# Kernel tuning notes

Measured on AMD Instinct MI355X. Metric: run time of the kernel, lower is better.

Reference implementation:

```python
import jax, jax.numpy as jnp
import numpy as np

D_MODEL = 1024
N_HEADS = 16
D_V = D_MODEL // N_HEADS  # 64


def setup_inputs() -> dict:
    key = jax.random.key(0)
    k1, k2, k3, k4, k5, k6 = jax.random.split(key, 6)
    N, L = 2, 2048
    return {
        "queries": jax.random.normal(k1, (N, L, D_MODEL), jnp.float32),
        "keys": jax.random.normal(k2, (N, L, D_MODEL), jnp.float32),
        "values": jax.random.normal(k3, (N, L, D_MODEL), jnp.float32),
        # key-padding mask, 0 = masked out (broadcast over heads and queries)
        "mask": jax.random.randint(k4, (N, 1, 1, L), 0, 2).astype(jnp.int32),
        # torch nn.Linear(d_model, d_model): weight [out, in], bias [out]
        "fc_w": jax.random.normal(k5, (D_MODEL, D_MODEL), jnp.float32) / np.sqrt(D_MODEL).astype(np.float32),
        "fc_b": jax.random.normal(k6, (D_MODEL,), jnp.float32) * 0.01,
    }


def reference(queries, keys, values, mask, fc_w, fc_b):
    N, Lq, _ = queries.shape
    Lk = keys.shape[1]
    # NOTE: the source defines Q/K/V Linear layers but never applies them in forward.
    q = queries.reshape(N, Lq, N_HEADS, D_V).transpose(0, 2, 1, 3)  # [N,H,Lq,Dv]
    k = keys.reshape(N, Lk, N_HEADS, D_V)                            # [N,Lk,H,Dv]
    v = values.reshape(N, Lk, N_HEADS, D_V)                          # [N,Lk,H,Dv]
    energy = jnp.einsum('nhqd,nkhd->nhqk', q, k)                     # QK^T
    energy = jnp.where(mask == 0, -jnp.inf, energy)                  # masked_fill
    # faithful to source: scale by sqrt(d_model), applied after masking
    attn = jax.nn.softmax(energy / jnp.sqrt(jnp.float32(D_MODEL)), axis=-1)
    out = jnp.einsum('nhqk,nkhd->nqhd', attn, v).reshape(N, Lq, N_HEADS * D_V)
    return out @ fc_w.T + fc_b
```

## Files before the change

### kernel.cpp

```cpp
#include <hip/hip_runtime.h>
#include <hip/hip_bf16.h>

#define SEQL 2048
#define DMODEL 1024

typedef short bf16x8 __attribute__((ext_vector_type(8)));
typedef short bf16x4 __attribute__((ext_vector_type(4)));
typedef float f32x4 __attribute__((ext_vector_type(4)));
typedef unsigned short u16;

__device__ __forceinline__ u16 f2bf(float f) {
    union { float f; unsigned u; } v; v.f = f;
    unsigned r = v.u + 0x7FFFu + ((v.u >> 16) & 1u);
    return (u16)(r >> 16);
}

__device__ __forceinline__ void async16(u16* lds, const u16* g) {
    __builtin_amdgcn_global_load_lds(
        (const __attribute__((address_space(1))) unsigned int*)g,
        (__attribute__((address_space(3))) unsigned int*)lds,
        16, 0, 0);
}


#define TSTR 72

__global__ __launch_bounds__(256) void pack_all(
    const float* __restrict__ kg, const float* __restrict__ wg,
    const float* __restrict__ vg, const int* __restrict__ mg,
    u16* __restrict__ kb, u16* __restrict__ wb, u16* __restrict__ vtb,
    float* __restrict__ maskf)
{
    __shared__ __align__(16) u16 T[64 * TSTR];
    const int b = blockIdx.x, t = threadIdx.x;
    u16 o[8];
    if (b < 2048) {
        const int e0 = (b * 256 + t) * 8;
        const int n = e0 >> 21;
        const int s = (e0 >> 10) & 2047;
        const int dm = e0 & 1023, h = dm >> 6, d0 = dm & 63;
        const float4 x0 = *(const float4*)(kg + e0);
        const float4 x1 = *(const float4*)(kg + e0 + 4);
        o[0]=f2bf(x0.x); o[1]=f2bf(x0.y); o[2]=f2bf(x0.z); o[3]=f2bf(x0.w);
        o[4]=f2bf(x1.x); o[5]=f2bf(x1.y); o[6]=f2bf(x1.z); o[7]=f2bf(x1.w);
        const int kt = s >> 6, st = (s >> 4) & 3, m = s & 15;
        const int f = d0 >> 5, qd = (d0 >> 3) & 3;
        u16* dst = kb + ((size_t)((n * 16 + h) * 32 + kt)) * 4096
                      + (st * 2 + f) * 512 + (m + 16 * qd) * 8;
        *(bf16x8*)dst = *(bf16x8*)o;
    } else if (b < 2560) {
        const int e0 = ((b - 2048) * 256 + t) * 8;
        const int col = e0 >> 10, k0 = e0 & 1023;
        const float4 x0 = *(const float4*)(wg + e0);
        const float4 x1 = *(const float4*)(wg + e0 + 4);
        o[0]=f2bf(x0.x); o[1]=f2bf(x0.y); o[2]=f2bf(x0.z); o[3]=f2bf(x0.w);
        o[4]=f2bf(x1.x); o[5]=f2bf(x1.y); o[6]=f2bf(x1.z); o[7]=f2bf(x1.w);
        const int cb = col >> 6, cj = (col >> 4) & 3, m = col & 15;
        const int kt = k0 >> 6, f = (k0 >> 5) & 1, qd = (k0 >> 3) & 3;
        u16* dst = wb + ((size_t)((cb * 16 + kt) * 8 + cj * 2 + f)) * 512
                      + (m + 16 * qd) * 8;
        *(bf16x8*)dst = *(bf16x8*)o;
    } else if (b < 3584) {
        const int bb = b - 2560;
        const int kt = bb & 31, h = (bb >> 5) & 15, n = bb >> 9;
        {
            const int s = t >> 2, d0 = (t & 3) * 16;
            const float* src = vg + ((size_t)(n * SEQL + kt * 64 + s) * DMODEL) + h * 64 + d0;
            u16 w16[16];
            #pragma unroll
            for (int j = 0; j < 16; ++j) w16[j] = f2bf(src[j]);
            *(bf16x8*)&T[s * TSTR + d0]     = *(bf16x8*)&w16[0];
            *(bf16x8*)&T[s * TSTR + d0 + 8] = *(bf16x8*)&w16[8];
        }
        __syncthreads();
        {
            const int d = t >> 2, k0 = (t & 3) * 16;
            u16 w16[16];
            #pragma unroll
            for (int j = 0; j < 16; ++j) w16[j] = T[(k0 + j) * TSTR + d];
            const int t4 = d >> 4, dr = d & 15;
            u16* base = vtb + ((size_t)((n * 16 + h) * 32 + kt)) * 4096;
            #pragma unroll
            for (int g = 0; g < 2; ++g) {
                const int key0 = k0 + g * 8;
                const int kk = key0 >> 5, qk = (key0 >> 3) & 3;
                *(bf16x8*)(base + (t4 * 2 + kk) * 512 + (dr + 16 * qk) * 8)
                    = *(bf16x8*)&w16[g * 8];
            }
        }
    } else {
        #pragma unroll
        for (int i = 0; i < 16; ++i) {
            const int idx = t * 16 + i;
            maskf[idx] = mg[idx] ? 0.0f : -1.0e5f;
        }
    }
}

#define OSPLIT 4194304
#define LSPLIT 65536

template<int NSPLIT>
__global__ __launch_bounds__(256) void attn_kernel(
    const float* __restrict__ qg, const u16* __restrict__ kb,
    const u16* __restrict__ vtb, const float* __restrict__ maskf,
    u16* __restrict__ xb, float* __restrict__ opart, float* __restrict__ lpart)
{
    __shared__ __align__(16) u16 SM[16384];
    u16* const K_lds = SM;
    u16* const V_lds = SM + 4096;
    u16* const P_lds = SM + 8192;

    const int blk = blockIdx.x;
    const int qblk = blk & 15;
    const int h = (blk >> 4) & 15;
    const int n = (blk >> 8) & 1;
    const int split = blk >> 9;
    const int tid = threadIdx.x;
    const int wave = tid >> 6, lane = tid & 63;
    const int lrow = lane & 15, quad = lane >> 4;
    const int q0 = qblk * 128;

    bf16x8 qf[2][2];
    #pragma unroll
    for (int qi = 0; qi < 2; ++qi) {
        const float* qp = qg + ((size_t)(n * SEQL + q0 + wave * 32 + qi * 16 + lrow) * DMODEL) + h * 64 + quad * 8;
        #pragma unroll
        for (int f = 0; f < 2; ++f) {
            const float4 a = *(const float4*)(qp + f * 32);
            const float4 c = *(const float4*)(qp + f * 32 + 4);
            u16* dst = (u16*)&qf[qi][f];
            dst[0]=f2bf(a.x); dst[1]=f2bf(a.y); dst[2]=f2bf(a.z); dst[3]=f2bf(a.w);
            dst[4]=f2bf(c.x); dst[5]=f2bf(c.y); dst[6]=f2bf(c.z); dst[7]=f2bf(c.w);
        }
    }

    bf16x8 onesf;
    #pragma unroll
    for (int j = 0; j < 8; ++j) ((u16*)&onesf)[j] = 0x3F80;

    f32x4 oacc[2][4];
    f32x4 lacc[2];
    #pragma unroll
    for (int qi = 0; qi < 2; ++qi) {
        lacc[qi] = (f32x4){0.f, 0.f, 0.f, 0.f};
        #pragma unroll
        for (int t4 = 0; t4 < 4; ++t4) oacc[qi][t4] = (f32x4){0.f, 0.f, 0.f, 0.f};
    }

    const u16* ksrc0 = kb  + ((size_t)(n * 16 + h)) * 131072;
    const u16* vsrc0 = vtb + ((size_t)(n * 16 + h)) * 131072;
    const float* mrow = maskf + n * SEQL;

    const int ktlo = split * (32 / NSPLIT);
    const int kthi = ktlo + (32 / NSPLIT);

    for (int kt = ktlo; kt < kthi; ++kt) {
        __syncthreads();
        {
            const u16* ks = ksrc0 + (size_t)kt * 4096;
            const u16* vs = vsrc0 + (size_t)kt * 4096;
            #pragma unroll
            for (int i = 0; i < 2; ++i) {
                const int ch = tid + i * 256;
                async16(&K_lds[ch * 8], ks + ch * 8);
                async16(&V_lds[ch * 8], vs + ch * 8);
            }
        }
        __syncthreads();

        #pragma unroll
        for (int st = 0; st < 4; ++st) {
            const bf16x8 kf0 = *(const bf16x8*)&K_lds[(st * 2 + 0) * 512 + lane * 8];
            const bf16x8 kf1 = *(const bf16x8*)&K_lds[(st * 2 + 1) * 512 + lane * 8];
            const f32x4 mv = *(const f32x4*)&mrow[kt * 64 + st * 16 + quad * 4];
            const int kk = st >> 1;
            const int qk = (st & 1) * 2 + (quad >> 1);
            const int j0 = (quad & 1) * 4;
            #pragma unroll
            for (int qi = 0; qi < 2; ++qi) {
                f32x4 sa = (f32x4){0.f, 0.f, 0.f, 0.f};
                sa = __builtin_amdgcn_mfma_f32_16x16x32_bf16(kf0, qf[qi][0], sa, 0, 0, 0);
                sa = __builtin_amdgcn_mfma_f32_16x16x32_bf16(kf1, qf[qi][1], sa, 0, 0, 0);
                float e0v = __expf(fmaf(sa[0], 0.03125f, mv[0]));
                float e1v = __expf(fmaf(sa[1], 0.03125f, mv[1]));
                float e2v = __expf(fmaf(sa[2], 0.03125f, mv[2]));
                float e3v = __expf(fmaf(sa[3], 0.03125f, mv[3]));
                __hip_bfloat162 h0 = __float22bfloat162_rn(make_float2(e0v, e1v));
                __hip_bfloat162 h1 = __float22bfloat162_rn(make_float2(e2v, e3v));
                union { unsigned u[2]; bf16x4 v; } pk;
                pk.u[0] = *(unsigned*)&h0;
                pk.u[1] = *(unsigned*)&h1;
                *(bf16x4*)&P_lds[wave * 2048 + (qi * 2 + kk) * 512 + (lrow + 16 * qk) * 8 + j0] = pk.v;
            }
        }
        asm volatile("s_waitcnt lgkmcnt(0)" ::: "memory");

        bf16x8 vf[4][2];
        #pragma unroll
        for (int t4 = 0; t4 < 4; ++t4) {
            vf[t4][0] = *(const bf16x8*)&V_lds[(t4 * 2 + 0) * 512 + lane * 8];
            vf[t4][1] = *(const bf16x8*)&V_lds[(t4 * 2 + 1) * 512 + lane * 8];
        }
        #pragma unroll
        for (int qi = 0; qi < 2; ++qi) {
            const bf16x8 pf0 = *(const bf16x8*)&P_lds[wave * 2048 + (qi * 2 + 0) * 512 + lane * 8];
            const bf16x8 pf1 = *(const bf16x8*)&P_lds[wave * 2048 + (qi * 2 + 1) * 512 + lane * 8];
            lacc[qi] = __builtin_amdgcn_mfma_f32_16x16x32_bf16(pf0, onesf, lacc[qi], 0, 0, 0);
            lacc[qi] = __builtin_amdgcn_mfma_f32_16x16x32_bf16(pf1, onesf, lacc[qi], 0, 0, 0);
            #pragma unroll
            for (int t4 = 0; t4 < 4; ++t4) {
                oacc[qi][t4] = __builtin_amdgcn_mfma_f32_16x16x32_bf16(pf0, vf[t4][0], oacc[qi][t4], 0, 0, 0);
                oacc[qi][t4] = __builtin_amdgcn_mfma_f32_16x16x32_bf16(pf1, vf[t4][1], oacc[qi][t4], 0, 0, 0);
            }
        }
    }

    if (NSPLIT == 1) {
        #pragma unroll
        for (int qi = 0; qi < 2; ++qi)
            #pragma unroll
            for (int r = 0; r < 4; ++r) {
                const float rinv = 1.0f / lacc[qi][r];
                const int row = n * SEQL + q0 + wave * 32 + qi * 16 + quad * 4 + r;
                const int rb = row >> 7, rt = (row >> 4) & 7, m = row & 15;
                #pragma unroll
                for (int t4 = 0; t4 < 4; ++t4) {
                    const int f = t4 >> 1;
                    const int qd = (t4 & 1) * 2 + (lrow >> 3);
                    xb[((size_t)((rb * 16 + h) * 16 + rt * 2 + f)) * 512
                       + (m + 16 * qd) * 8 + (lrow & 7)] = f2bf(oacc[qi][t4][r] * rinv);
                }
            }
    } else {
        #pragma unroll
        for (int qi = 0; qi < 2; ++qi) {
            #pragma unroll
            for (int r = 0; r < 4; ++r) {
                const int q = q0 + wave * 32 + qi * 16 + quad * 4 + r;
                float* op = opart + (size_t)split * OSPLIT + (size_t)(n * SEQL + q) * DMODEL + h * 64 + lrow;
                #pragma unroll
                for (int t4 = 0; t4 < 4; ++t4)
                    op[t4 * 16] = oacc[qi][t4][r];
                if (lrow == 0)
                    lpart[split * LSPLIT + (n * SEQL + q) * 16 + h] = lacc[qi][r];
            }
        }
    }
}

template<int NSPLIT>
__global__ __launch_bounds__(256) void reduce_norm(
    const float* __restrict__ opart, const float* __restrict__ lpart,
    u16* __restrict__ xb)
{
    const int gid = blockIdx.x * 256 + threadIdx.x;
    const int e0 = gid * 8;
    const int row = e0 >> 10, k0 = e0 & 1023, h = k0 >> 6;
    float lsum = 0.f;
    #pragma unroll
    for (int s = 0; s < NSPLIT; ++s) lsum += lpart[s * LSPLIT + row * 16 + h];
    const float rinv = 1.0f / lsum;
    float a[8] = {0.f,0.f,0.f,0.f,0.f,0.f,0.f,0.f};
    #pragma unroll
    for (int s = 0; s < NSPLIT; ++s) {
        const float4 x0 = *(const float4*)(opart + (size_t)s * OSPLIT + e0);
        const float4 x1 = *(const float4*)(opart + (size_t)s * OSPLIT + e0 + 4);
        a[0]+=x0.x; a[1]+=x0.y; a[2]+=x0.z; a[3]+=x0.w;
        a[4]+=x1.x; a[5]+=x1.y; a[6]+=x1.z; a[7]+=x1.w;
    }
    u16 o[8];
    #pragma unroll
    for (int j = 0; j < 8; ++j) o[j] = f2bf(a[j] * rinv);
    const int rb = row >> 7, rt = (row >> 4) & 7, m = row & 15;
    const int kt = k0 >> 6, f = (k0 >> 5) & 1, qd = (k0 >> 3) & 3;
    *(bf16x8*)(xb + ((size_t)((rb * 16 + kt) * 16 + rt * 2 + f)) * 512
                  + (m + 16 * qd) * 8) = *(bf16x8*)o;
}

__global__ __launch_bounds__(256) void fc_kernel(
    const u16* __restrict__ xb, const u16* __restrict__ wb,
    const float* __restrict__ bias, float* __restrict__ out)
{
    __shared__ __align__(16) u16 SM[12288];
    u16* const X_lds = SM;
    u16* const W_lds = SM + 8192;

    const int blk = blockIdx.x;
    const int cb = blk & 15, rb = blk >> 4;
    const int tid = threadIdx.x;
    const int wave = tid >> 6, lane = tid & 63;
    const int lrow = lane & 15, quad = lane >> 4;

    f32x4 acc[2][4];
    #pragma unroll
    for (int ri = 0; ri < 2; ++ri)
        #pragma unroll
        for (int cj = 0; cj < 4; ++cj) acc[ri][cj] = (f32x4){0.f, 0.f, 0.f, 0.f};

    for (int kt = 0; kt < 16; ++kt) {
        __syncthreads();
        {
            const u16* xs = xb + ((size_t)(rb * 16 + kt)) * 8192;
            const u16* ws = wb + ((size_t)(cb * 16 + kt)) * 4096;
            #pragma unroll
            for (int i = 0; i < 4; ++i) {
                const int ch = tid + i * 256;
                async16(&X_lds[ch * 8], xs + ch * 8);
            }
            #pragma unroll
            for (int i = 0; i < 2; ++i) {
                const int ch = tid + i * 256;
                async16(&W_lds[ch * 8], ws + ch * 8);
            }
        }
        __syncthreads();

        bf16x8 af[2][2];
        #pragma unroll
        for (int ri = 0; ri < 2; ++ri) {
            af[ri][0] = *(const bf16x8*)&X_lds[((wave * 2 + ri) * 2 + 0) * 512 + lane * 8];
            af[ri][1] = *(const bf16x8*)&X_lds[((wave * 2 + ri) * 2 + 1) * 512 + lane * 8];
        }
        #pragma unroll
        for (int cj = 0; cj < 4; ++cj) {
            const bf16x8 bf0 = *(const bf16x8*)&W_lds[(cj * 2 + 0) * 512 + lane * 8];
            const bf16x8 bf1 = *(const bf16x8*)&W_lds[(cj * 2 + 1) * 512 + lane * 8];
            #pragma unroll
            for (int ri = 0; ri < 2; ++ri) {
                acc[ri][cj] = __builtin_amdgcn_mfma_f32_16x16x32_bf16(af[ri][0], bf0, acc[ri][cj], 0, 0, 0);
                acc[ri][cj] = __builtin_amdgcn_mfma_f32_16x16x32_bf16(af[ri][1], bf1, acc[ri][cj], 0, 0, 0);
            }
        }
    }

    const int row0 = rb * 128, col0 = cb * 64;
    #pragma unroll
    for (int ri = 0; ri < 2; ++ri)
        #pragma unroll
        for (int cj = 0; cj < 4; ++cj) {
            const int col = col0 + cj * 16 + lrow;
            const float bv = bias[col];
            #pragma unroll
            for (int r = 0; r < 4; ++r)
                out[(size_t)(row0 + wave * 32 + ri * 16 + quad * 4 + r) * DMODEL + col] = acc[ri][cj][r] + bv;
        }
}

extern "C" void kernel_launch(void* const* d_in, const int* in_sizes, int n_in,
                              void* d_out, int out_size, void* d_ws, size_t ws_size,
                              hipStream_t stream) {
    const float* q   = (const float*)d_in[0];
    const float* k   = (const float*)d_in[1];
    const float* v   = (const float*)d_in[2];
    const int*   m   = (const int*)d_in[3];
    const float* fcw = (const float*)d_in[4];
    const float* fcb = (const float*)d_in[5];
    float* out = (float*)d_out;

    char* ws = (char*)d_ws;
    u16*   kbuf  = (u16*)(ws);
    u16*   vtbuf = (u16*)(ws + (8u  << 20));
    u16*   wbuf  = (u16*)(ws + (16u << 20));
    u16*   xbuf  = (u16*)(ws + (18u << 20));
    float* maskf = (float*)(ws + (26u << 20));
    float* opart = (float*)(ws + (27u << 20));
    float* lpart = (float*)(ws + (59u << 20));
    const bool split2 = ws_size >= (60u << 20);

    pack_all<<<dim3(3585), dim3(256), 0, stream>>>(k, fcw, v, m, kbuf, wbuf, vtbuf, maskf);
    if (split2) {
        attn_kernel<2><<<dim3(1024), dim3(256), 0, stream>>>(q, kbuf, vtbuf, maskf, xbuf, opart, lpart);
        reduce_norm<2><<<dim3(2048), dim3(256), 0, stream>>>(opart, lpart, xbuf);
    } else {
        attn_kernel<1><<<dim3(512), dim3(256), 0, stream>>>(q, kbuf, vtbuf, maskf, xbuf, opart, lpart);
    }
    fc_kernel<<<dim3(512), dim3(256), 0, stream>>>(xbuf, wbuf, fcb, out);
}
```

Before: 185.3 us.

## Double-buffer K/V and X/W LDS tiles; use exp2 with prescaled log2e

Both the attention and FC kernels now keep two LDS buffers. The first tile is loaded before the loop, and each iteration prefetches the next tile into the other buffer before running the MFMA work on the current one, with a single barrier at the end of each iteration. The goal is to hide global-to-LDS latency behind compute. The softmax exponent now uses a hardware exp2 with the scale multiplied by log2(e), which saves a multiply per element. In exchange, LDS use per block grows to 48KB, which can lower the number of resident blocks per CU.

```diff
diff --git a/kernel.cpp b/kernel.cpp
--- a/kernel.cpp
+++ b/kernel.cpp
@@ -14,6 +14,16 @@
     unsigned r = v.u + 0x7FFFu + ((v.u >> 16) & 1u);
     return (u16)(r >> 16);
 }
+
+__device__ __forceinline__ float fexp2(float x) {
+#if __has_builtin(__builtin_amdgcn_exp2f)
+    return __builtin_amdgcn_exp2f(x);
+#else
+    return exp2f(x);
+#endif
+}
+
+#define SCALE2 0.04508422f
 
 __device__ __forceinline__ void async16(u16* lds, const u16* g) {
     __builtin_amdgcn_global_load_lds(
@@ -106,10 +116,10 @@
     const u16* __restrict__ vtb, const float* __restrict__ maskf,
     u16* __restrict__ xb, float* __restrict__ opart, float* __restrict__ lpart)
 {
-    __shared__ __align__(16) u16 SM[16384];
+    __shared__ __align__(16) u16 SM[24576];
     u16* const K_lds = SM;
-    u16* const V_lds = SM + 4096;
-    u16* const P_lds = SM + 8192;
+    u16* const V_lds = SM + 8192;
+    u16* const P_lds = SM + 16384;
 
     const int blk = blockIdx.x;
     const int qblk = blk & 15;
@@ -121,6 +131,24 @@
     const int lrow = lane & 15, quad = lane >> 4;
     const int q0 = qblk * 128;
 
+    const u16* ksrc0 = kb  + ((size_t)(n * 16 + h)) * 131072;
+    const u16* vsrc0 = vtb + ((size_t)(n * 16 + h)) * 131072;
+    const float* mrow = maskf + n * SEQL;
+
+    const int ktlo = split * (32 / NSPLIT);
+    const int kthi = ktlo + (32 / NSPLIT);
+
+    {
+        const u16* ks = ksrc0 + (size_t)ktlo * 4096;
+        const u16* vs = vsrc0 + (size_t)ktlo * 4096;
+        #pragma unroll
+        for (int i = 0; i < 2; ++i) {
+            const int ch = tid + i * 256;
+            async16(&K_lds[ch * 8], ks + ch * 8);
+            async16(&V_lds[ch * 8], vs + ch * 8);
+        }
+    }
+
     bf16x8 qf[2][2];
     #pragma unroll
     for (int qi = 0; qi < 2; ++qi) {
@@ -148,31 +176,29 @@
         for (int t4 = 0; t4 < 4; ++t4) oacc[qi][t4] = (f32x4){0.f, 0.f, 0.f, 0.f};
     }
 
-    const u16* ksrc0 = kb  + ((size_t)(n * 16 + h)) * 131072;
-    const u16* vsrc0 = vtb + ((size_t)(n * 16 + h)) * 131072;
-    const float* mrow = maskf + n * SEQL;
-
-    const int ktlo = split * (32 / NSPLIT);
-    const int kthi = ktlo + (32 / NSPLIT);
+    __syncthreads();
 
     for (int kt = ktlo; kt < kthi; ++kt) {
-        __syncthreads();
-        {
-            const u16* ks = ksrc0 + (size_t)kt * 4096;
-            const u16* vs = vsrc0 + (size_t)kt * 4096;
+        const int cur = (kt - ktlo) & 1;
+        const u16* const Kc = K_lds + cur * 4096;
+        const u16* const Vc = V_lds + cur * 4096;
+
+        if (kt + 1 < kthi) {
+            const int nxt = cur ^ 1;
+            const u16* ks = ksrc0 + (size_t)(kt + 1) * 4096;
+            const u16* vs = vsrc0 + (size_t)(kt + 1) * 4096;
             #pragma unroll
             for (int i = 0; i < 2; ++i) {
                 const int ch = tid + i * 256;
-                async16(&K_lds[ch * 8], ks + ch * 8);
-                async16(&V_lds[ch * 8], vs + ch * 8);
-            }
-        }
-        __syncthreads();
+                async16(&K_lds[nxt * 4096 + ch * 8], ks + ch * 8);
+                async16(&V_lds[nxt * 4096 + ch * 8], vs + ch * 8);
+            }
+        }
 
         #pragma unroll
         for (int st = 0; st < 4; ++st) {
-            const bf16x8 kf0 = *(const bf16x8*)&K_lds[(st * 2 + 0) * 512 + lane * 8];
-            const bf16x8 kf1 = *(const bf16x8*)&K_lds[(st * 2 + 1) * 512 + lane * 8];
+            const bf16x8 kf0 = *(const bf16x8*)&Kc[(st * 2 + 0) * 512 + lane * 8];
+            const bf16x8 kf1 = *(const bf16x8*)&Kc[(st * 2 + 1) * 512 + lane * 8];
             const f32x4 mv = *(const f32x4*)&mrow[kt * 64 + st * 16 + quad * 4];
             const int kk = st >> 1;
             const int qk = (st & 1) * 2 + (quad >> 1);
@@ -182,10 +208,10 @@
                 f32x4 sa = (f32x4){0.f, 0.f, 0.f, 0.f};
                 sa = __builtin_amdgcn_mfma_f32_16x16x32_bf16(kf0, qf[qi][0], sa, 0, 0, 0);
                 sa = __builtin_amdgcn_mfma_f32_16x16x32_bf16(kf1, qf[qi][1], sa, 0, 0, 0);
-                float e0v = __expf(fmaf(sa[0], 0.03125f, mv[0]));
-                float e1v = __expf(fmaf(sa[1], 0.03125f, mv[1]));
-                float e2v = __expf(fmaf(sa[2], 0.03125f, mv[2]));
-                float e3v = __expf(fmaf(sa[3], 0.03125f, mv[3]));
+                float e0v = fexp2(fmaf(sa[0], SCALE2, mv[0]));
+                float e1v = fexp2(fmaf(sa[1], SCALE2, mv[1]));
+                float e2v = fexp2(fmaf(sa[2], SCALE2, mv[2]));
+                float e3v = fexp2(fmaf(sa[3], SCALE2, mv[3]));
                 __hip_bfloat162 h0 = __float22bfloat162_rn(make_float2(e0v, e1v));
                 __hip_bfloat162 h1 = __float22bfloat162_rn(make_float2(e2v, e3v));
                 union { unsigned u[2]; bf16x4 v; } pk;
@@ -199,8 +225,8 @@
         bf16x8 vf[4][2];
         #pragma unroll
         for (int t4 = 0; t4 < 4; ++t4) {
-            vf[t4][0] = *(const bf16x8*)&V_lds[(t4 * 2 + 0) * 512 + lane * 8];
-            vf[t4][1] = *(const bf16x8*)&V_lds[(t4 * 2 + 1) * 512 + lane * 8];
+            vf[t4][0] = *(const bf16x8*)&Vc[(t4 * 2 + 0) * 512 + lane * 8];
+            vf[t4][1] = *(const bf16x8*)&Vc[(t4 * 2 + 1) * 512 + lane * 8];
         }
         #pragma unroll
         for (int qi = 0; qi < 2; ++qi) {
@@ -214,6 +240,8 @@
                 oacc[qi][t4] = __builtin_amdgcn_mfma_f32_16x16x32_bf16(pf1, vf[t4][1], oacc[qi][t4], 0, 0, 0);
             }
         }
+
+        __syncthreads();
     }
 
     if (NSPLIT == 1) {
@@ -282,9 +310,9 @@
     const u16* __restrict__ xb, const u16* __restrict__ wb,
     const float* __restrict__ bias, float* __restrict__ out)
 {
-    __shared__ __align__(16) u16 SM[12288];
+    __shared__ __align__(16) u16 SM[24576];
     u16* const X_lds = SM;
-    u16* const W_lds = SM + 8192;
+    u16* const W_lds = SM + 16384;
 
     const int blk = blockIdx.x;
     const int cb = blk & 15, rb = blk >> 4;
@@ -292,46 +320,68 @@
     const int wave = tid >> 6, lane = tid & 63;
     const int lrow = lane & 15, quad = lane >> 4;
 
+    const u16* xs0 = xb + ((size_t)rb * 16) * 8192;
+    const u16* ws0 = wb + ((size_t)cb * 16) * 4096;
+
     f32x4 acc[2][4];
     #pragma unroll
     for (int ri = 0; ri < 2; ++ri)
         #pragma unroll
         for (int cj = 0; cj < 4; ++cj) acc[ri][cj] = (f32x4){0.f, 0.f, 0.f, 0.f};
 
+    {
+        #pragma unroll
+        for (int i = 0; i < 4; ++i) {
+            const int ch = tid + i * 256;
+            async16(&X_lds[ch * 8], xs0 + ch * 8);
+        }
+        #pragma unroll
+        for (int i = 0; i < 2; ++i) {
+            const int ch = tid + i * 256;
+            async16(&W_lds[ch * 8], ws0 + ch * 8);
+        }
+    }
+    __syncthreads();
+
     for (int kt = 0; kt < 16; ++kt) {
-        __syncthreads();
-        {
-            const u16* xs = xb + ((size_t)(rb * 16 + kt)) * 8192;
-            const u16* ws = wb + ((size_t)(cb * 16 + kt)) * 4096;
+        const int cur = kt & 1;
+        const u16* const Xc = X_lds + cur * 8192;
+        const u16* const Wc = W_lds + cur * 4096;
+
+        if (kt + 1 < 16) {
+            const int nxt = cur ^ 1;
+            const u16* xs = xs0 + (size_t)(kt + 1) * 8192;
+            const u16* ws = ws0 + (size_t)(kt + 1) * 4096;
             #pragma unroll
             for (int i = 0; i < 4; ++i) {
                 const int ch = tid + i * 256;
-                async16(&X_lds[ch * 8], xs + ch * 8);
+                async16(&X_lds[nxt * 8192 + ch * 8], xs + ch * 8);
             }
             #pragma unroll
             for (int i = 0; i < 2; ++i) {
                 const int ch = tid + i * 256;
-                async16(&W_lds[ch * 8], ws + ch * 8);
-            }
-        }
-        __syncthreads();
+                async16(&W_lds[nxt * 4096 + ch * 8], ws + ch * 8);
+            }
+        }
 
         bf16x8 af[2][2];
         #pragma unroll
         for (int ri = 0; ri < 2; ++ri) {
-            af[ri][0] = *(const bf16x8*)&X_lds[((wave * 2 + ri) * 2 + 0) * 512 + lane * 8];
-            af[ri][1] = *(const bf16x8*)&X_lds[((wave * 2 + ri) * 2 + 1) * 512 + lane * 8];
+            af[ri][0] = *(const bf16x8*)&Xc[((wave * 2 + ri) * 2 + 0) * 512 + lane * 8];
+            af[ri][1] = *(const bf16x8*)&Xc[((wave * 2 + ri) * 2 + 1) * 512 + lane * 8];
         }
         #pragma unroll
         for (int cj = 0; cj < 4; ++cj) {
-            const bf16x8 bf0 = *(const bf16x8*)&W_lds[(cj * 2 + 0) * 512 + lane * 8];
-            const bf16x8 bf1 = *(const bf16x8*)&W_lds[(cj * 2 + 1) * 512 + lane * 8];
+            const bf16x8 bf0 = *(const bf16x8*)&Wc[(cj * 2 + 0) * 512 + lane * 8];
+            const bf16x8 bf1 = *(const bf16x8*)&Wc[(cj * 2 + 1) * 512 + lane * 8];
             #pragma unroll
             for (int ri = 0; ri < 2; ++ri) {
                 acc[ri][cj] = __builtin_amdgcn_mfma_f32_16x16x32_bf16(af[ri][0], bf0, acc[ri][cj], 0, 0, 0);
                 acc[ri][cj] = __builtin_amdgcn_mfma_f32_16x16x32_bf16(af[ri][1], bf1, acc[ri][cj], 0, 0, 0);
             }
         }
+
+        __syncthreads();
     }
 
     const int row0 = rb * 128, col0 = cb * 64;
```

New measurement: 182.1 us. About the same (-1.8%).
